# Kernel tuning notes

Hardware: AMD Instinct MI355X
Metric: run time of the kernel (lower is better)

Reference implementation:

```python
import jax, jax.numpy as jnp
import numpy as np

N = 50000      # num nodes
IN = 256       # in_channels
H = 4          # heads
C = 64         # out_channels per head (concat=False -> out_dim = C)
HOPS = 3       # max_hops == num hops provided
E = 400000     # edges per hop
NEG_SLOPE = 0.2


def setup_inputs() -> dict:
    key = jax.random.key(0)
    ks = jax.random.split(key, 10)
    s_in = 1.0 / np.sqrt(IN)
    s_c = 1.0 / np.sqrt(C)
    return {
        "x": jax.random.normal(ks[0], (N, IN), jnp.float32),
        "ei0": jax.random.randint(ks[1], (2, E), 0, N, dtype=jnp.int32),
        "ei1": jax.random.randint(ks[2], (2, E), 0, N, dtype=jnp.int32),
        "ei2": jax.random.randint(ks[3], (2, E), 0, N, dtype=jnp.int32),
        # shared left/right projections (lin_l / lin_r, shared across hops)
        "W_l": jax.random.normal(ks[4], (IN, H * C), jnp.float32) * s_in,
        "b_l": jnp.zeros((H * C,), jnp.float32),
        "W_r": jax.random.normal(ks[5], (IN, H * C), jnp.float32) * s_in,
        "b_r": jnp.zeros((H * C,), jnp.float32),
        # hop-specific attention vectors and output biases
        "att": jax.random.normal(ks[6], (HOPS, H, C), jnp.float32) * s_c,
        "bias": jnp.zeros((HOPS, C), jnp.float32),
        # hop gate (single Linear since gate_hidden=None)
        "W_gate": jax.random.normal(ks[7], (IN, HOPS), jnp.float32) * s_in,
        "b_gate": jnp.zeros((HOPS,), jnp.float32),
    }


def _segment_softmax(logits, seg, n):
    # logits: [E, H], seg: [E] destination node ids
    m = jax.ops.segment_max(logits, seg, num_segments=n)          # [N, H]
    m = jnp.where(jnp.isfinite(m), m, 0.0)                        # empty segments -> 0
    ex = jnp.exp(logits - m[seg])
    s = jax.ops.segment_sum(ex, seg, num_segments=n)              # [N, H]
    return ex / (s[seg] + 1e-16)


def _gatv2_hop(x_l, x_r, edge_index, att_k, bias_k):
    # x_l, x_r: [N, H, C] shared projections; edge_index: [2, Ek]
    src, dst = edge_index[0], edge_index[1]
    s = jax.nn.leaky_relu(x_l[src] + x_r[dst], NEG_SLOPE)         # [Ek, H, C]
    alpha = jnp.einsum("ehc,hc->eh", s, att_k)                    # [Ek, H]
    alpha = _segment_softmax(alpha, dst, N)
    msg = jax.ops.segment_sum(x_l[src] * alpha[..., None], dst, num_segments=N)  # [N, H, C]
    return msg.mean(axis=1) + bias_k                              # concat=False -> head mean, [N, C]


def reference(x, ei0, ei1, ei2, W_l, b_l, W_r, b_r, att, bias, W_gate, b_gate):
    # shared projections computed once
    x_l = (x @ W_l + b_l).reshape(N, H, C)
    x_r = (x @ W_r + b_r).reshape(N, H, C)

    # hop 0 gets self-loops (add_self_loops=True); higher hops do not
    ar = jnp.arange(N, dtype=ei0.dtype)
    ei0_sl = jnp.concatenate([ei0, jnp.stack([ar, ar])], axis=1)
    edges = [ei0_sl, ei1, ei2]

    messages = jnp.stack(
        [_gatv2_hop(x_l, x_r, edges[k], att[k], bias[k]) for k in range(HOPS)],
        axis=1,
    )  # [N, HOPS, C]

    logits = x @ W_gate + b_gate                                  # [N, HOPS]
    weights = jax.nn.softmax(logits, axis=-1)
    out = jnp.einsum("nkc,nk->nc", messages, weights)             # [N, C]
    return out
```

## Files before the change

### kernel.cpp

```cpp
#include <hip/hip_runtime.h>
#include <math.h>

#define N_NODES 50000
#define IN_DIM 256
#define HEADS 4
#define CDIM 64
#define HC 256
#define HOPS 3
#define EDGES 400000
#define NEG_SLOPE 0.2f
#define SEG (EDGES + N_NODES)
#define TOT_E (3 * EDGES + N_NODES)
#define CAP 40

#define NB_GATE  ((N_NODES + 3) / 4)
#define NB_PACKW ((IN_DIM * 2 * HC) / 256)
#define NB_SCAT  ((TOT_E + 255) / 256)
#define GEMM_BX  ((N_NODES + 127) / 128)

typedef unsigned short ushort;
using short8  = __attribute__((ext_vector_type(8))) short;
using floatx4 = __attribute__((ext_vector_type(4))) float;

__device__ __forceinline__ void decode_flat(int f, int& k, int& e)
{
    if (f < SEG)              { k = 0; e = f; }
    else if (f < SEG + EDGES) { k = 1; e = f - SEG; }
    else                      { k = 2; e = f - SEG - EDGES; }
}

__device__ __forceinline__ ushort f2bf(float f)
{
    unsigned u = __float_as_uint(f);
    unsigned r = u + 0x7fffu + ((u >> 16) & 1u);
    return (ushort)(r >> 16);
}

__global__ __launch_bounds__(256) void prep(
    const float* __restrict__ X, const float* __restrict__ Wg,
    const float* __restrict__ bg, float* __restrict__ gw,
    ushort* __restrict__ Xb,
    const float* __restrict__ Wl, const float* __restrict__ Wr,
    ushort* __restrict__ WT,
    const int* __restrict__ ei0, const int* __restrict__ ei1,
    const int* __restrict__ ei2, int* __restrict__ cnt,
    int* __restrict__ bucket)
{
    const int blk = blockIdx.x;
    const int tid = threadIdx.x;

    if (blk < NB_GATE) {
        const int node = (blk * 256 + tid) >> 6;
        const int lane = tid & 63;
        if (node >= N_NODES) return;

        float4 xv = ((const float4*)(X + (size_t)node * IN_DIM))[lane];

        union { ushort s[4]; uint2 u; } o;
        o.s[0] = f2bf(xv.x); o.s[1] = f2bf(xv.y);
        o.s[2] = f2bf(xv.z); o.s[3] = f2bf(xv.w);
        ((uint2*)(Xb + (size_t)node * IN_DIM))[lane] = o.u;

        float a0 = 0.f, a1 = 0.f, a2 = 0.f;
        const int i0 = lane * 4;
        a0 += xv.x * Wg[(i0 + 0) * HOPS + 0]; a1 += xv.x * Wg[(i0 + 0) * HOPS + 1]; a2 += xv.x * Wg[(i0 + 0) * HOPS + 2];
        a0 += xv.y * Wg[(i0 + 1) * HOPS + 0]; a1 += xv.y * Wg[(i0 + 1) * HOPS + 1]; a2 += xv.y * Wg[(i0 + 1) * HOPS + 2];
        a0 += xv.z * Wg[(i0 + 2) * HOPS + 0]; a1 += xv.z * Wg[(i0 + 2) * HOPS + 1]; a2 += xv.z * Wg[(i0 + 2) * HOPS + 2];
        a0 += xv.w * Wg[(i0 + 3) * HOPS + 0]; a1 += xv.w * Wg[(i0 + 3) * HOPS + 1]; a2 += xv.w * Wg[(i0 + 3) * HOPS + 2];

        #pragma unroll
        for (int off = 32; off >= 1; off >>= 1) {
            a0 += __shfl_xor(a0, off);
            a1 += __shfl_xor(a1, off);
            a2 += __shfl_xor(a2, off);
        }
        if (lane == 0) {
            float l0 = a0 + bg[0], l1 = a1 + bg[1], l2 = a2 + bg[2];
            float m = fmaxf(l0, fmaxf(l1, l2));
            float e0 = expf(l0 - m), e1 = expf(l1 - m), e2 = expf(l2 - m);
            float inv = 1.f / (e0 + e1 + e2);
            gw[node * HOPS + 0] = e0 * inv;
            gw[node * HOPS + 1] = e1 * inv;
            gw[node * HOPS + 2] = e2 * inv;
        }
    } else if (blk < NB_GATE + NB_PACKW) {
        int id = (blk - NB_GATE) * 256 + tid;
        int n = id >> 8;
        int k = id & 255;
        float v = (n < HC) ? Wl[k * HC + n] : Wr[k * HC + (n - HC)];
        WT[(size_t)n * IN_DIM + k] = f2bf(v);
    } else {
        int f = (blk - NB_GATE - NB_PACKW) * 256 + tid;
        if (f >= TOT_E) return;
        int k, e; decode_flat(f, k, e);
        int s, d;
        if (k == 0 && e >= EDGES) { s = d = e - EDGES; }
        else {
            const int* ei = (k == 0) ? ei0 : (k == 1) ? ei1 : ei2;
            s = ei[e]; d = ei[EDGES + e];
        }
        int pos = atomicAdd(&cnt[k * N_NODES + d], 1);
        if (pos < CAP)
            bucket[((size_t)k * N_NODES + d) * CAP + pos] = s;
    }
}

#define TM 128
#define TN 128
#define TK 32
#define LDP 40

__global__ __launch_bounds__(256) void gemm_mfma(
    const ushort* __restrict__ Xb, const ushort* __restrict__ WT,
    const float* __restrict__ b_l, const float* __restrict__ b_r,
    ushort* __restrict__ xlb, ushort* __restrict__ xrb, int M)
{
    __shared__ ushort As[TM][LDP];
    __shared__ ushort Bs[TN][LDP];
    const int tid  = threadIdx.x;
    const int wave = tid >> 6, lane = tid & 63;
    const int row0 = blockIdx.x * TM;
    const int col0 = blockIdx.y * TN;
    const int wy = (wave >> 1) * 64, wx = (wave & 1) * 64;
    const int lrow = lane & 15, lk = (lane >> 4) * 8;

    floatx4 acc[4][4];
    #pragma unroll
    for (int i = 0; i < 4; i++)
        #pragma unroll
        for (int j = 0; j < 4; j++)
            acc[i][j] = (floatx4){0.f, 0.f, 0.f, 0.f};

    for (int k0 = 0; k0 < IN_DIM; k0 += TK) {
        #pragma unroll
        for (int j = 0; j < 2; j++) {
            int id = tid + 256 * j;
            int r  = id >> 2;
            int c  = (id & 3) * 8;
            int gr = row0 + r;
            uint4 v = make_uint4(0u, 0u, 0u, 0u);
            if (gr < M)
                v = *(const uint4*)(Xb + (size_t)gr * IN_DIM + k0 + c);
            *(uint4*)&As[r][c] = v;
        }
        #pragma unroll
        for (int j = 0; j < 2; j++) {
            int id = tid + 256 * j;
            int r  = id >> 2;
            int c  = (id & 3) * 8;
            *(uint4*)&Bs[r][c] =
                *(const uint4*)(WT + (size_t)(col0 + r) * IN_DIM + k0 + c);
        }
        __syncthreads();

        short8 af[4], bf[4];
        #pragma unroll
        for (int mi = 0; mi < 4; mi++)
            af[mi] = *(const short8*)&As[wy + mi * 16 + lrow][lk];
        #pragma unroll
        for (int ni = 0; ni < 4; ni++)
            bf[ni] = *(const short8*)&Bs[wx + ni * 16 + lrow][lk];

        #pragma unroll
        for (int mi = 0; mi < 4; mi++)
            #pragma unroll
            for (int ni = 0; ni < 4; ni++)
                acc[mi][ni] = __builtin_amdgcn_mfma_f32_16x16x32_bf16(
                    bf[ni], af[mi], acc[mi][ni], 0, 0, 0);
        __syncthreads();
    }

    const int csub = (lane >> 4) * 4;
    #pragma unroll
    for (int mi = 0; mi < 4; mi++) {
        int grow = row0 + wy + mi * 16 + lrow;
        if (grow < M) {
            #pragma unroll
            for (int ni = 0; ni < 4; ni++) {
                int gcol = col0 + wx + ni * 16 + csub;
                floatx4 v = acc[mi][ni];
                const bool left = (gcol < HC);
                const float4 b = left ? *(const float4*)(b_l + gcol)
                                      : *(const float4*)(b_r + gcol - HC);
                union { ushort s[4]; uint2 u; } o;
                o.s[0] = f2bf(v[0] + b.x);
                o.s[1] = f2bf(v[1] + b.y);
                o.s[2] = f2bf(v[2] + b.z);
                o.s[3] = f2bf(v[3] + b.w);
                ushort* dst = left ? (xlb + (size_t)grow * HC + gcol)
                                   : (xrb + (size_t)grow * HC + gcol - HC);
                *(uint2*)dst = o.u;
            }
        }
    }
}

__global__ __launch_bounds__(192) void node_all(
    const ushort* __restrict__ xlb, const ushort* __restrict__ xrb,
    const int* __restrict__ cnt, const int* __restrict__ bucket,
    const float* __restrict__ att, const float* __restrict__ gw,
    const float* __restrict__ bias, float* __restrict__ out)
{
    __shared__ float lds[HOPS][CDIM];
    const int n    = blockIdx.x;
    const int k    = threadIdx.x >> 6;
    const int lane = threadIdx.x & 63;
    const int half = lane >> 5;
    const int sub  = lane & 31;

    const int deg = min(cnt[k * N_NODES + n], CAP);
    const int* bk = bucket + ((size_t)k * N_NODES + n) * CAP;

    uint4 rq = *(const uint4*)(xrb + (size_t)n * HC + sub * 8);
    const float rr0 = __uint_as_float(rq.x << 16);
    const float rr1 = __uint_as_float(rq.x & 0xffff0000u);
    const float rr2 = __uint_as_float(rq.y << 16);
    const float rr3 = __uint_as_float(rq.y & 0xffff0000u);
    const float rr4 = __uint_as_float(rq.z << 16);
    const float rr5 = __uint_as_float(rq.z & 0xffff0000u);
    const float rr6 = __uint_as_float(rq.w << 16);
    const float rr7 = __uint_as_float(rq.w & 0xffff0000u);

    const float4 wa = ((const float4*)(att + (size_t)k * HC))[sub * 2 + 0];
    const float4 wb = ((const float4*)(att + (size_t)k * HC))[sub * 2 + 1];

    float denom = 0.f;
    float acc[8] = {0.f, 0.f, 0.f, 0.f, 0.f, 0.f, 0.f, 0.f};

    if (deg > 0) {
        int myS = (lane < deg) ? bk[lane] : 0;
        const int npair = (deg + 1) >> 1;

        int s0 = __shfl(myS, min(half, deg - 1));
        uint4 q = *(const uint4*)(xlb + (size_t)s0 * HC + sub * 8);

        for (int j = 0; j < npair; j++) {
            int idxn = min(2 * (j + 1) + half, deg - 1);
            int sn = __shfl(myS, idxn);
            uint4 qn = *(const uint4*)(xlb + (size_t)sn * HC + sub * 8);

            float f0 = __uint_as_float(q.x << 16);
            float f1 = __uint_as_float(q.x & 0xffff0000u);
            float f2 = __uint_as_float(q.y << 16);
            float f3 = __uint_as_float(q.y & 0xffff0000u);
            float f4 = __uint_as_float(q.z << 16);
            float f5 = __uint_as_float(q.z & 0xffff0000u);
            float f6 = __uint_as_float(q.w << 16);
            float f7 = __uint_as_float(q.w & 0xffff0000u);

            float v0 = f0 + rr0, v1 = f1 + rr1, v2 = f2 + rr2, v3 = f3 + rr3;
            float v4 = f4 + rr4, v5 = f5 + rr5, v6 = f6 + rr6, v7 = f7 + rr7;

            float p;
            p = 0.6f * wa.x * v0 + 0.4f * wa.x * fabsf(v0);
            p = fmaf(0.6f * wa.y, v1, p); p = fmaf(0.4f * wa.y, fabsf(v1), p);
            p = fmaf(0.6f * wa.z, v2, p); p = fmaf(0.4f * wa.z, fabsf(v2), p);
            p = fmaf(0.6f * wa.w, v3, p); p = fmaf(0.4f * wa.w, fabsf(v3), p);
            p = fmaf(0.6f * wb.x, v4, p); p = fmaf(0.4f * wb.x, fabsf(v4), p);
            p = fmaf(0.6f * wb.y, v5, p); p = fmaf(0.4f * wb.y, fabsf(v5), p);
            p = fmaf(0.6f * wb.z, v6, p); p = fmaf(0.4f * wb.z, fabsf(v6), p);
            p = fmaf(0.6f * wb.w, v7, p); p = fmaf(0.4f * wb.w, fabsf(v7), p);

            p += __shfl_xor(p, 1);
            p += __shfl_xor(p, 2);
            p += __shfl_xor(p, 4);

            bool valid = (2 * j + half) < deg;
            float ex = valid ? __expf(p) : 0.f;
            denom += ex;
            acc[0] = fmaf(ex, f0, acc[0]);
            acc[1] = fmaf(ex, f1, acc[1]);
            acc[2] = fmaf(ex, f2, acc[2]);
            acc[3] = fmaf(ex, f3, acc[3]);
            acc[4] = fmaf(ex, f4, acc[4]);
            acc[5] = fmaf(ex, f5, acc[5]);
            acc[6] = fmaf(ex, f6, acc[6]);
            acc[7] = fmaf(ex, f7, acc[7]);
            q = qn;
        }
    }

    denom += __shfl_xor(denom, 32);
    #pragma unroll
    for (int i = 0; i < 8; i++) acc[i] += __shfl_xor(acc[i], 32);

    float inv = (denom > 0.f) ? 1.f / denom : 0.f;
    const float g  = gw[n * HOPS + k];
    const float* bb = bias + (size_t)k * CDIM + (sub & 7) * 8;

    #pragma unroll
    for (int i = 0; i < 8; i++) {
        float v = acc[i] * inv;
        v += __shfl_xor(v, 8);
        v += __shfl_xor(v, 16);
        if (lane < 8) lds[k][lane * 8 + i] = g * (v * 0.25f + bb[i]);
    }
    __syncthreads();

    if (threadIdx.x < CDIM)
        out[(size_t)n * CDIM + threadIdx.x] =
            lds[0][threadIdx.x] + lds[1][threadIdx.x] + lds[2][threadIdx.x];
}

extern "C" void kernel_launch(void* const* d_in, const int* in_sizes, int n_in,
                              void* d_out, int out_size, void* d_ws, size_t ws_size,
                              hipStream_t stream)
{
    const float* x      = (const float*)d_in[0];
    const int*   ei0    = (const int*)d_in[1];
    const int*   ei1    = (const int*)d_in[2];
    const int*   ei2    = (const int*)d_in[3];
    const float* W_l    = (const float*)d_in[4];
    const float* b_l    = (const float*)d_in[5];
    const float* W_r    = (const float*)d_in[6];
    const float* b_r    = (const float*)d_in[7];
    const float* att    = (const float*)d_in[8];
    const float* bias   = (const float*)d_in[9];
    const float* W_gate = (const float*)d_in[10];
    const float* b_gate = (const float*)d_in[11];

    const size_t NHC = (size_t)N_NODES * HC;
    float* ws      = (float*)d_ws;
    float* gwbuf   = ws;
    int*   cnt     = (int*)(gwbuf + HOPS * N_NODES);
    int*   bucket  = cnt + HOPS * N_NODES;
    ushort* xlb    = (ushort*)(bucket + (size_t)HOPS * N_NODES * CAP);
    ushort* xrb    = xlb + NHC;
    ushort* Xb     = xrb + NHC;
    ushort* WT     = Xb + NHC;

    hipMemsetAsync(cnt, 0, (size_t)HOPS * N_NODES * sizeof(int), stream);

    prep<<<NB_GATE + NB_PACKW + NB_SCAT, 256, 0, stream>>>(
        x, W_gate, b_gate, gwbuf, Xb, W_l, W_r, WT,
        ei0, ei1, ei2, cnt, bucket);

    dim3 ggrid(GEMM_BX, 4);
    gemm_mfma<<<ggrid, 256, 0, stream>>>(Xb, WT, b_l, b_r, xlb, xrb, N_NODES);

    node_all<<<N_NODES, 192, 0, stream>>>(
        xlb, xrb, cnt, bucket, att, gwbuf, bias, (float*)d_out);
}
```

Before: 399.5 us.

## Fuse GEMM with prep kernel, converting fp32 inputs to bf16 on the fly

Merges the projection GEMM into the prep kernel as extra blocks, loading fp32 X and W directly and converting to bf16 while staging into LDS. This drops the intermediate Xb/WT buffers and one kernel launch, and lets the GEMM run alongside the gate and edge-bucketing work. In exchange, each GEMM block reads X in fp32 four times over (once per column tile) and does strided W transposition in shared memory. The node kernel also simplifies its neighbor-index clamping by loading a clamped bucket slot.

After: 413.5 us. +3.5%, slower.

```diff
diff --git a/kernel.cpp b/kernel.cpp
--- a/kernel.cpp
+++ b/kernel.cpp
@@ -1,4 +1,5 @@
 #include <hip/hip_runtime.h>
+#include <hip/hip_bf16.h>
 #include <math.h>
 
 #define N_NODES 50000
@@ -13,10 +14,15 @@
 #define TOT_E (3 * EDGES + N_NODES)
 #define CAP 40
 
+#define TM 128
+#define TN 128
+#define TK 32
+#define LDP 40
+#define GEMM_BX  ((N_NODES + TM - 1) / TM)
+
+#define NB_GEMM  (GEMM_BX * 4)
 #define NB_GATE  ((N_NODES + 3) / 4)
-#define NB_PACKW ((IN_DIM * 2 * HC) / 256)
 #define NB_SCAT  ((TOT_E + 255) / 256)
-#define GEMM_BX  ((N_NODES + 127) / 128)
 
 typedef unsigned short ushort;
 using short8  = __attribute__((ext_vector_type(8))) short;
@@ -36,30 +42,131 @@
     return (ushort)(r >> 16);
 }
 
-__global__ __launch_bounds__(256) void prep(
-    const float* __restrict__ X, const float* __restrict__ Wg,
-    const float* __restrict__ bg, float* __restrict__ gw,
-    ushort* __restrict__ Xb,
+__device__ __forceinline__ unsigned pk2(float a, float b)
+{
+    __hip_bfloat162 h = __float22bfloat162_rn(make_float2(a, b));
+    union { __hip_bfloat162 h; unsigned u; } c;
+    c.h = h;
+    return c.u;
+}
+
+__global__ __launch_bounds__(256) void mega(
+    const float* __restrict__ X,
     const float* __restrict__ Wl, const float* __restrict__ Wr,
-    ushort* __restrict__ WT,
+    const float* __restrict__ b_l, const float* __restrict__ b_r,
+    ushort* __restrict__ xlb, ushort* __restrict__ xrb, int M,
+    const float* __restrict__ Wg, const float* __restrict__ bg,
+    float* __restrict__ gw,
     const int* __restrict__ ei0, const int* __restrict__ ei1,
     const int* __restrict__ ei2, int* __restrict__ cnt,
     int* __restrict__ bucket)
 {
+    __shared__ ushort As[TM][LDP];
+    __shared__ ushort Bs[TN][LDP];
     const int blk = blockIdx.x;
     const int tid = threadIdx.x;
 
-    if (blk < NB_GATE) {
-        const int node = (blk * 256 + tid) >> 6;
+    if (blk < NB_GEMM) {
+        const int wave = tid >> 6, lane = tid & 63;
+        const int row0 = (blk % GEMM_BX) * TM;
+        const int col0 = (blk / GEMM_BX) * TN;
+        const int wy = (wave >> 1) * 64, wx = (wave & 1) * 64;
+        const int lrow = lane & 15, lk = (lane >> 4) * 8;
+
+        const bool left = (col0 < HC);
+        const float* Wsrc = left ? (Wl + col0) : (Wr + col0 - HC);
+
+        floatx4 acc[4][4];
+        #pragma unroll
+        for (int i = 0; i < 4; i++)
+            #pragma unroll
+            for (int j = 0; j < 4; j++)
+                acc[i][j] = (floatx4){0.f, 0.f, 0.f, 0.f};
+
+        for (int k0 = 0; k0 < IN_DIM; k0 += TK) {
+            {
+                const int r  = tid >> 1;
+                const int cb = (tid & 1) * 16;
+                const int gr = row0 + r;
+                float4 v0 = {0,0,0,0}, v1 = {0,0,0,0}, v2 = {0,0,0,0}, v3 = {0,0,0,0};
+                if (gr < M) {
+                    const float4* px = (const float4*)(X + (size_t)gr * IN_DIM + k0 + cb);
+                    v0 = px[0]; v1 = px[1]; v2 = px[2]; v3 = px[3];
+                }
+                uint4 ua, ub;
+                ua.x = pk2(v0.x, v0.y); ua.y = pk2(v0.z, v0.w);
+                ua.z = pk2(v1.x, v1.y); ua.w = pk2(v1.z, v1.w);
+                ub.x = pk2(v2.x, v2.y); ub.y = pk2(v2.z, v2.w);
+                ub.z = pk2(v3.x, v3.y); ub.w = pk2(v3.z, v3.w);
+                *(uint4*)&As[r][cb + 0] = ua;
+                *(uint4*)&As[r][cb + 8] = ub;
+            }
+            {
+                const int kp = tid >> 4;
+                const int nb = (tid & 15) * 8;
+                const int kr = k0 + 2 * kp;
+                const float* w0 = Wsrc + (size_t)kr * HC + nb;
+                const float* w1 = w0 + HC;
+                float4 a0 = *(const float4*)(w0 + 0);
+                float4 a1 = *(const float4*)(w0 + 4);
+                float4 b0 = *(const float4*)(w1 + 0);
+                float4 b1 = *(const float4*)(w1 + 4);
+                *(unsigned*)&Bs[nb + 0][2 * kp] = pk2(a0.x, b0.x);
+                *(unsigned*)&Bs[nb + 1][2 * kp] = pk2(a0.y, b0.y);
+                *(unsigned*)&Bs[nb + 2][2 * kp] = pk2(a0.z, b0.z);
+                *(unsigned*)&Bs[nb + 3][2 * kp] = pk2(a0.w, b0.w);
+                *(unsigned*)&Bs[nb + 4][2 * kp] = pk2(a1.x, b1.x);
+                *(unsigned*)&Bs[nb + 5][2 * kp] = pk2(a1.y, b1.y);
+                *(unsigned*)&Bs[nb + 6][2 * kp] = pk2(a1.z, b1.z);
+                *(unsigned*)&Bs[nb + 7][2 * kp] = pk2(a1.w, b1.w);
+            }
+            __syncthreads();
+
+            short8 af[4], bf[4];
+            #pragma unroll
+            for (int mi = 0; mi < 4; mi++)
+                af[mi] = *(const short8*)&As[wy + mi * 16 + lrow][lk];
+            #pragma unroll
+            for (int ni = 0; ni < 4; ni++)
+                bf[ni] = *(const short8*)&Bs[wx + ni * 16 + lrow][lk];
+
+            #pragma unroll
+            for (int mi = 0; mi < 4; mi++)
+                #pragma unroll
+                for (int ni = 0; ni < 4; ni++)
+                    acc[mi][ni] = __builtin_amdgcn_mfma_f32_16x16x32_bf16(
+                        bf[ni], af[mi], acc[mi][ni], 0, 0, 0);
+            __syncthreads();
+        }
+
+        const int csub = (lane >> 4) * 4;
+        ushort* dstbuf = left ? xlb : xrb;
+        const float* bvec = left ? b_l : b_r;
+        const int cbase = left ? col0 : col0 - HC;
+        #pragma unroll
+        for (int mi = 0; mi < 4; mi++) {
+            int grow = row0 + wy + mi * 16 + lrow;
+            if (grow < M) {
+                #pragma unroll
+                for (int ni = 0; ni < 4; ni++) {
+                    int gcol = cbase + wx + ni * 16 + csub;
+                    floatx4 v = acc[mi][ni];
+                    const float4 b = *(const float4*)(bvec + gcol);
+                    union { ushort s[4]; uint2 u; } o;
+                    o.s[0] = f2bf(v[0] + b.x);
+                    o.s[1] = f2bf(v[1] + b.y);
+                    o.s[2] = f2bf(v[2] + b.z);
+                    o.s[3] = f2bf(v[3] + b.w);
+                    *(uint2*)(dstbuf + (size_t)grow * HC + gcol) = o.u;
+                }
+            }
+        }
+    } else if (blk < NB_GEMM + NB_GATE) {
+        const int node = ((blk - NB_GEMM) * 256 + tid) >> 6;
         const int lane = tid & 63;
         if (node >= N_NODES) return;
 
         float4 xv = ((const float4*)(X + (size_t)node * IN_DIM))[lane];
-
-        union { ushort s[4]; uint2 u; } o;
-        o.s[0] = f2bf(xv.x); o.s[1] = f2bf(xv.y);
-        o.s[2] = f2bf(xv.z); o.s[3] = f2bf(xv.w);
-        ((uint2*)(Xb + (size_t)node * IN_DIM))[lane] = o.u;
 
         float a0 = 0.f, a1 = 0.f, a2 = 0.f;
         const int i0 = lane * 4;
@@ -83,14 +190,8 @@
             gw[node * HOPS + 1] = e1 * inv;
             gw[node * HOPS + 2] = e2 * inv;
         }
-    } else if (blk < NB_GATE + NB_PACKW) {
-        int id = (blk - NB_GATE) * 256 + tid;
-        int n = id >> 8;
-        int k = id & 255;
-        float v = (n < HC) ? Wl[k * HC + n] : Wr[k * HC + (n - HC)];
-        WT[(size_t)n * IN_DIM + k] = f2bf(v);
     } else {
-        int f = (blk - NB_GATE - NB_PACKW) * 256 + tid;
+        int f = (blk - NB_GEMM - NB_GATE) * 256 + tid;
         if (f >= TOT_E) return;
         int k, e; decode_flat(f, k, e);
         int s, d;
@@ -102,96 +203,6 @@
         int pos = atomicAdd(&cnt[k * N_NODES + d], 1);
         if (pos < CAP)
             bucket[((size_t)k * N_NODES + d) * CAP + pos] = s;
-    }
-}
-
-#define TM 128
-#define TN 128
-#define TK 32
-#define LDP 40
-
-__global__ __launch_bounds__(256) void gemm_mfma(
-    const ushort* __restrict__ Xb, const ushort* __restrict__ WT,
-    const float* __restrict__ b_l, const float* __restrict__ b_r,
-    ushort* __restrict__ xlb, ushort* __restrict__ xrb, int M)
-{
-    __shared__ ushort As[TM][LDP];
-    __shared__ ushort Bs[TN][LDP];
-    const int tid  = threadIdx.x;
-    const int wave = tid >> 6, lane = tid & 63;
-    const int row0 = blockIdx.x * TM;
-    const int col0 = blockIdx.y * TN;
-    const int wy = (wave >> 1) * 64, wx = (wave & 1) * 64;
-    const int lrow = lane & 15, lk = (lane >> 4) * 8;
-
-    floatx4 acc[4][4];
-    #pragma unroll
-    for (int i = 0; i < 4; i++)
-        #pragma unroll
-        for (int j = 0; j < 4; j++)
-            acc[i][j] = (floatx4){0.f, 0.f, 0.f, 0.f};
-
-    for (int k0 = 0; k0 < IN_DIM; k0 += TK) {
-        #pragma unroll
-        for (int j = 0; j < 2; j++) {
-            int id = tid + 256 * j;
-            int r  = id >> 2;
-            int c  = (id & 3) * 8;
-            int gr = row0 + r;
-            uint4 v = make_uint4(0u, 0u, 0u, 0u);
-            if (gr < M)
-                v = *(const uint4*)(Xb + (size_t)gr * IN_DIM + k0 + c);
-            *(uint4*)&As[r][c] = v;
-        }
-        #pragma unroll
-        for (int j = 0; j < 2; j++) {
-            int id = tid + 256 * j;
-            int r  = id >> 2;
-            int c  = (id & 3) * 8;
-            *(uint4*)&Bs[r][c] =
-                *(const uint4*)(WT + (size_t)(col0 + r) * IN_DIM + k0 + c);
-        }
-        __syncthreads();
-
-        short8 af[4], bf[4];
-        #pragma unroll
-        for (int mi = 0; mi < 4; mi++)
-            af[mi] = *(const short8*)&As[wy + mi * 16 + lrow][lk];
-        #pragma unroll
-        for (int ni = 0; ni < 4; ni++)
-            bf[ni] = *(const short8*)&Bs[wx + ni * 16 + lrow][lk];
-
-        #pragma unroll
-        for (int mi = 0; mi < 4; mi++)
-            #pragma unroll
-            for (int ni = 0; ni < 4; ni++)
-                acc[mi][ni] = __builtin_amdgcn_mfma_f32_16x16x32_bf16(
-                    bf[ni], af[mi], acc[mi][ni], 0, 0, 0);
-        __syncthreads();
-    }
-
-    const int csub = (lane >> 4) * 4;
-    #pragma unroll
-    for (int mi = 0; mi < 4; mi++) {
-        int grow = row0 + wy + mi * 16 + lrow;
-        if (grow < M) {
-            #pragma unroll
-            for (int ni = 0; ni < 4; ni++) {
-                int gcol = col0 + wx + ni * 16 + csub;
-                floatx4 v = acc[mi][ni];
-                const bool left = (gcol < HC);
-                const float4 b = left ? *(const float4*)(b_l + gcol)
-                                      : *(const float4*)(b_r + gcol - HC);
-                union { ushort s[4]; uint2 u; } o;
-                o.s[0] = f2bf(v[0] + b.x);
-                o.s[1] = f2bf(v[1] + b.y);
-                o.s[2] = f2bf(v[2] + b.z);
-                o.s[3] = f2bf(v[3] + b.w);
-                ushort* dst = left ? (xlb + (size_t)grow * HC + gcol)
-                                   : (xrb + (size_t)grow * HC + gcol - HC);
-                *(uint2*)dst = o.u;
-            }
-        }
     }
 }
 
@@ -228,14 +239,14 @@
     float acc[8] = {0.f, 0.f, 0.f, 0.f, 0.f, 0.f, 0.f, 0.f};
 
     if (deg > 0) {
-        int myS = (lane < deg) ? bk[lane] : 0;
+        int myS = bk[lane < deg ? lane : deg - 1];
         const int npair = (deg + 1) >> 1;
 
-        int s0 = __shfl(myS, min(half, deg - 1));
+        int s0 = __shfl(myS, half);
         uint4 q = *(const uint4*)(xlb + (size_t)s0 * HC + sub * 8);
 
         for (int j = 0; j < npair; j++) {
-            int idxn = min(2 * (j + 1) + half, deg - 1);
+            int idxn = 2 * (j + 1) + half;
             int sn = __shfl(myS, idxn);
             uint4 qn = *(const uint4*)(xlb + (size_t)sn * HC + sub * 8);
 
@@ -326,17 +337,12 @@
     int*   bucket  = cnt + HOPS * N_NODES;
     ushort* xlb    = (ushort*)(bucket + (size_t)HOPS * N_NODES * CAP);
     ushort* xrb    = xlb + NHC;
-    ushort* Xb     = xrb + NHC;
-    ushort* WT     = Xb + NHC;
 
     hipMemsetAsync(cnt, 0, (size_t)HOPS * N_NODES * sizeof(int), stream);
 
-    prep<<<NB_GATE + NB_PACKW + NB_SCAT, 256, 0, stream>>>(
-        x, W_gate, b_gate, gwbuf, Xb, W_l, W_r, WT,
-        ei0, ei1, ei2, cnt, bucket);
-
-    dim3 ggrid(GEMM_BX, 4);
-    gemm_mfma<<<ggrid, 256, 0, stream>>>(Xb, WT, b_l, b_r, xlb, xrb, N_NODES);
+    mega<<<NB_GEMM + NB_GATE + NB_SCAT, 256, 0, stream>>>(
+        x, W_l, W_r, b_l, b_r, xlb, xrb, N_NODES,
+        W_gate, b_gate, gwbuf, ei0, ei1, ei2, cnt, bucket);
 
     node_all<<<N_NODES, 192, 0, stream>>>(
         xlb, xrb, cnt, bucket, att, gwbuf, bias, (float*)d_out);
```
